# Kernel tuning notes

Hardware: AMD Instinct MI355X
Metric: run time of the kernel (lower is better)

The kernel has to match this reference:

```python
import jax, jax.numpy as jnp
import numpy as np

DIM = 4096
N_HEADS = 32
N_KV_HEADS = 8
HEAD_DIM = DIM // N_HEADS  # 128
N_REP = N_HEADS // N_KV_HEADS  # 4
MAX_BS = 16
MAX_SEQ = 4096
SEQLEN = 1
START_POS = 4095
ROPE_THETA = 500000.0


def setup_inputs() -> dict:
    key = jax.random.key(0)
    ks = jax.random.split(key, 8)
    w_scale = 0.02  # keep logits in a sane range
    x = jax.random.normal(ks[0], (MAX_BS, SEQLEN, DIM), dtype=jnp.float32)
    wq = jax.random.normal(ks[1], (DIM, N_HEADS * HEAD_DIM), dtype=jnp.float32) * w_scale
    wk = jax.random.normal(ks[2], (DIM, N_KV_HEADS * HEAD_DIM), dtype=jnp.float32) * w_scale
    wv = jax.random.normal(ks[3], (DIM, N_KV_HEADS * HEAD_DIM), dtype=jnp.float32) * w_scale
    wo = jax.random.normal(ks[4], (N_HEADS * HEAD_DIM, DIM), dtype=jnp.float32) * w_scale
    cache_k = jax.random.normal(ks[5], (MAX_BS, MAX_SEQ, N_KV_HEADS, HEAD_DIM), dtype=jnp.float32)
    cache_v = jax.random.normal(ks[6], (MAX_BS, MAX_SEQ, N_KV_HEADS, HEAD_DIM), dtype=jnp.float32)
    # true rotary frequencies for positions [START_POS, START_POS+SEQLEN)
    inv_freq = 1.0 / (ROPE_THETA ** (np.arange(0, HEAD_DIM, 2, dtype=np.float32) / HEAD_DIM))  # [hd/2]
    t = np.arange(START_POS, START_POS + SEQLEN, dtype=np.float32)[:, None]  # [s,1]
    angles = t * inv_freq[None, :]  # [s, hd/2]
    freqs_cos = jnp.asarray(np.cos(angles), dtype=jnp.float32)
    freqs_sin = jnp.asarray(np.sin(angles), dtype=jnp.float32)
    return {"x": x, "wq": wq, "wk": wk, "wv": wv, "wo": wo,
            "cache_k": cache_k, "cache_v": cache_v,
            "freqs_cos": freqs_cos, "freqs_sin": freqs_sin,
            "start_pos": START_POS}


def _rope(t, cos, sin):
    # t: [b, s, h, hd]; cos/sin: [s, hd/2] -> broadcast [1, s, 1, hd/2]
    b, s, h, hd = t.shape
    tp = t.reshape(b, s, h, hd // 2, 2)
    e, o = tp[..., 0], tp[..., 1]
    c = cos[None, :, None, :]
    sn = sin[None, :, None, :]
    re = e * c - o * sn
    im = e * sn + o * c
    return jnp.stack([re, im], axis=-1).reshape(b, s, h, hd)


def reference(x, wq, wk, wv, wo, cache_k, cache_v, freqs_cos, freqs_sin, start_pos):
    bsz, seqlen, _ = x.shape
    xq = (x @ wq).reshape(bsz, seqlen, N_HEADS, HEAD_DIM)
    xk = (x @ wk).reshape(bsz, seqlen, N_KV_HEADS, HEAD_DIM)
    xv = (x @ wv).reshape(bsz, seqlen, N_KV_HEADS, HEAD_DIM)
    xq = _rope(xq, freqs_cos, freqs_sin)
    xk = _rope(xk, freqs_cos, freqs_sin)
    # KV-cache append
    cache_k = jax.lax.dynamic_update_slice(cache_k, xk, (0, start_pos, 0, 0))
    cache_v = jax.lax.dynamic_update_slice(cache_v, xv, (0, start_pos, 0, 0))
    kv_len = start_pos + seqlen  # static Python int
    keys = cache_k[:, :kv_len]    # [b, t, g, hd]
    values = cache_v[:, :kv_len]  # [b, t, g, hd]
    # GQA via broadcasting (math-equivalent to repeat_kv)
    q = xq.reshape(bsz, seqlen, N_KV_HEADS, N_REP, HEAD_DIM)
    scale = 1.0 / jnp.sqrt(jnp.float32(HEAD_DIM))
    scores = jnp.einsum('bsgrh,btgh->bgrst', q, keys) * scale  # [b,g,r,s,t]
    probs = jax.nn.softmax(scores.astype(jnp.float32), axis=-1).astype(xq.dtype)
    out = jnp.einsum('bgrst,btgh->bsgrh', probs, values)  # [b,s,g,r,hd]
    out = out.reshape(bsz, seqlen, N_HEADS * HEAD_DIM)
    return out @ wo
```

## Files before the change

### kernel.cpp

```cpp
#include <hip/hip_runtime.h>
#include <math.h>

#define DIM    4096
#define NH     32
#define NKV    8
#define HD     128
#define BS     16
#define KVLEN  4096
#define LASTPOS 4095
#define QKV_COLS 6144
#define NKC    64

typedef float f32x4 __attribute__((ext_vector_type(4)));

#define WS_QKV   0
#define WS_ATTN  98304
#define WS_PART  163840
#define WS_PQ    4489216
#define WS_PW    10780672

__global__ __launch_bounds__(256) void qkv_projA(
    const float* __restrict__ x, const float* __restrict__ wq,
    const float* __restrict__ wk, const float* __restrict__ wv,
    float* __restrict__ pq) {
  __shared__ float xs[16 * 64];
  const int tid = threadIdx.x;
  const int col = (blockIdx.x * 256 + tid) * 2;
  const int kc = blockIdx.y;
  const int k0 = kc * 64;

  for (int i = tid; i < 1024; i += 256) {
    int b = i >> 6, k = i & 63;
    xs[i] = x[b * DIM + k0 + k];
  }
  __syncthreads();

  const float* w;
  int wstride, wcol;
  if (col < 4096)      { w = wq; wstride = 4096; wcol = col; }
  else if (col < 5120) { w = wk; wstride = 1024; wcol = col - 4096; }
  else                 { w = wv; wstride = 1024; wcol = col - 5120; }
  const float* wp = w + (size_t)k0 * wstride + wcol;

  float acc0[16], acc1[16];
#pragma unroll
  for (int b = 0; b < 16; ++b) { acc0[b] = 0.f; acc1[b] = 0.f; }

#pragma unroll 2
  for (int k = 0; k < 64; k += 4) {
    float2 w0 = *(const float2*)(wp + (size_t)(k + 0) * wstride);
    float2 w1 = *(const float2*)(wp + (size_t)(k + 1) * wstride);
    float2 w2 = *(const float2*)(wp + (size_t)(k + 2) * wstride);
    float2 w3 = *(const float2*)(wp + (size_t)(k + 3) * wstride);
#pragma unroll
    for (int b = 0; b < 16; ++b) {
      float4 xb = *(const float4*)(&xs[b * 64 + k]);
      acc0[b] += xb.x * w0.x + xb.y * w1.x + xb.z * w2.x + xb.w * w3.x;
      acc1[b] += xb.x * w0.y + xb.y * w1.y + xb.z * w2.y + xb.w * w3.y;
    }
  }
#pragma unroll
  for (int b = 0; b < 16; ++b) {
    *(float2*)(&pq[((size_t)kc * 16 + b) * QKV_COLS + col]) = make_float2(acc0[b], acc1[b]);
  }
}

__global__ __launch_bounds__(256) void qkv_projB(
    const float* __restrict__ pq, float* __restrict__ qkv,
    const float* __restrict__ fc, const float* __restrict__ fs) {
  int t = blockIdx.x * 256 + threadIdx.x;
  int b = t / 3072, pr = t % 3072;
  int col = 2 * pr;
  float e = 0.f, o = 0.f;
#pragma unroll 8
  for (int kc = 0; kc < NKC; ++kc) {
    float2 v = *(const float2*)(&pq[((size_t)kc * 16 + b) * QKV_COLS + col]);
    e += v.x; o += v.y;
  }
  float re = e, im = o;
  if (col < 5120) {
    int i = (col & 127) >> 1;
    float c = fc[i], s = fs[i];
    float scale = (col < 4096) ? 0.08838834764831845f : 1.0f;
    re = (e * c - o * s) * scale;
    im = (e * s + o * c) * scale;
  }
  *(float2*)(&qkv[b * QKV_COLS + col]) = make_float2(re, im);
}

__global__ __launch_bounds__(256) void attn_partial(
    const float* __restrict__ cache_k, const float* __restrict__ cache_v,
    const float* __restrict__ qkv, float* __restrict__ part) {
  const int tid = threadIdx.x;
  const int w = tid >> 6, lane = tid & 63;
  const int p2 = lane >> 5, ql = lane & 31;
  const int chunk = blockIdx.x & 15;
  const int bg = blockIdx.x >> 4;
  const int b = bg >> 3, g = bg & 7;
  const int t0 = chunk * 256 + w * 64;

  const float* qbase = qkv + b * QKV_COLS + g * 512;
  f32x4 qh[4];
#pragma unroll
  for (int h = 0; h < 4; ++h) qh[h] = *(const f32x4*)(qbase + h * 128 + ql * 4);

  const float* kw = cache_k + (size_t)b * 4194304 + g * 128 + (size_t)t0 * 1024;
  const float* vw = cache_v + (size_t)b * 4194304 + g * 128 + (size_t)t0 * 1024;
  const float* xk = qkv + b * QKV_COLS + 4096 + g * 128;
  const float* xv = qkv + b * QKV_COLS + 5120 + g * 128;

  float m[4], l[4];
  f32x4 acc[4];
#pragma unroll
  for (int h = 0; h < 4; ++h) { m[h] = -1e30f; l[h] = 0.f; acc[h] = (f32x4)(0.f); }

  const bool haslast = (t0 + 63 == LASTPOS);

  for (int bt = 0; bt < 8; ++bt) {
    const float* kb8 = kw + bt * 8192;
    const float* vb8 = vw + bt * 8192;
    f32x4 kf[4], vf[4];
    if (!haslast || bt < 7) {
#pragma unroll
      for (int j = 0; j < 4; ++j)
        kf[j] = *(const f32x4*)(kb8 + (2 * j + p2) * 1024 + ql * 4);
#pragma unroll
      for (int j = 0; j < 4; ++j)
        vf[j] = *(const f32x4*)(vb8 + (2 * j + p2) * 1024 + ql * 4);
    } else {
#pragma unroll
      for (int j = 0; j < 4; ++j) {
        int t = t0 + 56 + 2 * j + p2;
        const float* kr = (t == LASTPOS) ? xk : (kb8 + (2 * j + p2) * 1024);
        kf[j] = *(const f32x4*)(kr + ql * 4);
      }
#pragma unroll
      for (int j = 0; j < 4; ++j) {
        int t = t0 + 56 + 2 * j + p2;
        const float* vr = (t == LASTPOS) ? xv : (vb8 + (2 * j + p2) * 1024);
        vf[j] = *(const f32x4*)(vr + ql * 4);
      }
    }

    float sv[4][4];
#pragma unroll
    for (int j = 0; j < 4; ++j) {
#pragma unroll
      for (int h = 0; h < 4; ++h) {
        f32x4 pr = kf[j] * qh[h];
        sv[j][h] = pr[0] + pr[1] + pr[2] + pr[3];
      }
    }
#pragma unroll
    for (int off = 1; off < 32; off <<= 1) {
#pragma unroll
      for (int j = 0; j < 4; ++j) {
#pragma unroll
        for (int h = 0; h < 4; ++h)
          sv[j][h] += __shfl_xor(sv[j][h], off);
      }
    }

#pragma unroll
    for (int h = 0; h < 4; ++h) {
      float bm = fmaxf(fmaxf(sv[0][h], sv[1][h]), fmaxf(sv[2][h], sv[3][h]));
      bm = fmaxf(bm, __shfl_xor(bm, 32));
      float mn = fmaxf(m[h], bm);
      float f = __expf(m[h] - mn);
      m[h] = mn;
      acc[h] *= f;
#pragma unroll
      for (int j = 0; j < 4; ++j) sv[j][h] = __expf(sv[j][h] - mn);
      float ls = sv[0][h] + sv[1][h] + sv[2][h] + sv[3][h];
      ls += __shfl_xor(ls, 32);
      l[h] = l[h] * f + ls;
    }

#pragma unroll
    for (int j = 0; j < 4; ++j) {
#pragma unroll
      for (int h = 0; h < 4; ++h) acc[h] += sv[j][h] * vf[j];
    }
  }

#pragma unroll
  for (int h = 0; h < 4; ++h) {
#pragma unroll
    for (int k = 0; k < 4; ++k) acc[h][k] += __shfl_xor(acc[h][k], 32);
  }

  const size_t u = (size_t)blockIdx.x * 4 + w;
  if (lane < 32) {
#pragma unroll
    for (int h = 0; h < 4; ++h)
      *(f32x4*)(&part[(u * 4 + h) * 132 + ql * 4]) = acc[h];
  }
  if (lane == 0) {
#pragma unroll
    for (int h = 0; h < 4; ++h) {
      part[(u * 4 + h) * 132 + 128] = m[h];
      part[(u * 4 + h) * 132 + 129] = l[h];
    }
  }
}

__global__ __launch_bounds__(256) void attn_combine(
    const float* __restrict__ part, float* __restrict__ attn_out) {
  int t = blockIdx.x * 256 + threadIdx.x;
  int d = t & 127, h = (t >> 7) & 3, g = (t >> 9) & 7, b = t >> 12;
  int bg = b * 8 + g;
  float M = -1e30f, num = 0.f, den = 0.f;
  for (int u = 0; u < 64; ++u) {
    const float* pr = part + ((size_t)(bg * 64 + u) * 4 + h) * 132;
    float mc = pr[128];
    float Mn = fmaxf(M, mc);
    float fo = __expf(M - Mn);
    float fcur = __expf(mc - Mn);
    num = num * fo + fcur * pr[d];
    den = den * fo + fcur * pr[129];
    M = Mn;
  }
  attn_out[b * DIM + (g * 4 + h) * 128 + d] = num / den;
}

__global__ __launch_bounds__(256) void out_projA(
    const float* __restrict__ attn, const float* __restrict__ wo,
    float* __restrict__ pw) {
  __shared__ float xs[16 * 64];
  const int tid = threadIdx.x;
  const int col = (blockIdx.x * 256 + tid) * 2;
  const int kc = blockIdx.y;
  const int k0 = kc * 64;

  for (int i = tid; i < 1024; i += 256) {
    int b = i >> 6, k = i & 63;
    xs[i] = attn[b * DIM + k0 + k];
  }
  __syncthreads();

  const float* wp = wo + (size_t)k0 * 4096 + col;
  float acc0[16], acc1[16];
#pragma unroll
  for (int b = 0; b < 16; ++b) { acc0[b] = 0.f; acc1[b] = 0.f; }

#pragma unroll 2
  for (int k = 0; k < 64; k += 4) {
    float2 w0 = *(const float2*)(wp + (size_t)(k + 0) * 4096);
    float2 w1 = *(const float2*)(wp + (size_t)(k + 1) * 4096);
    float2 w2 = *(const float2*)(wp + (size_t)(k + 2) * 4096);
    float2 w3 = *(const float2*)(wp + (size_t)(k + 3) * 4096);
#pragma unroll
    for (int b = 0; b < 16; ++b) {
      float4 xb = *(const float4*)(&xs[b * 64 + k]);
      acc0[b] += xb.x * w0.x + xb.y * w1.x + xb.z * w2.x + xb.w * w3.x;
      acc1[b] += xb.x * w0.y + xb.y * w1.y + xb.z * w2.y + xb.w * w3.y;
    }
  }
#pragma unroll
  for (int b = 0; b < 16; ++b) {
    *(float2*)(&pw[((size_t)kc * 16 + b) * DIM + col]) = make_float2(acc0[b], acc1[b]);
  }
}

__global__ __launch_bounds__(256) void out_projB(
    const float* __restrict__ pw, float* __restrict__ out) {
  int t = blockIdx.x * 256 + threadIdx.x;
  int b = t >> 12, col = t & 4095;
  float sum = 0.f;
#pragma unroll 8
  for (int kc = 0; kc < NKC; ++kc)
    sum += pw[((size_t)kc * 16 + b) * DIM + col];
  out[b * DIM + col] = sum;
}

extern "C" void kernel_launch(void* const* d_in, const int* in_sizes, int n_in,
                              void* d_out, int out_size, void* d_ws, size_t ws_size,
                              hipStream_t stream) {
  const float* x  = (const float*)d_in[0];
  const float* wq = (const float*)d_in[1];
  const float* wk = (const float*)d_in[2];
  const float* wv = (const float*)d_in[3];
  const float* wo = (const float*)d_in[4];
  const float* ck = (const float*)d_in[5];
  const float* cv = (const float*)d_in[6];
  const float* fc = (const float*)d_in[7];
  const float* fs = (const float*)d_in[8];

  float* ws_f  = (float*)d_ws;
  float* qkv   = ws_f + WS_QKV;
  float* attn  = ws_f + WS_ATTN;
  float* part  = ws_f + WS_PART;
  float* pq    = ws_f + WS_PQ;
  float* pw    = ws_f + WS_PW;
  float* out   = (float*)d_out;

  qkv_projA<<<dim3(12, NKC), 256, 0, stream>>>(x, wq, wk, wv, pq);
  qkv_projB<<<192, 256, 0, stream>>>(pq, qkv, fc, fs);
  attn_partial<<<2048, 256, 0, stream>>>(ck, cv, qkv, part);
  attn_combine<<<256, 256, 0, stream>>>(part, attn);
  out_projA<<<dim3(8, NKC), 256, 0, stream>>>(attn, wo, pw);
  out_projB<<<256, 256, 0, stream>>>(pw, out);
}
```

Before: 205.4 us.

## Double-buffer KV loads and reduce warp partials in shared memory before combine

The attention partial kernel now prefetches the next K/V tile into a second register buffer while it computes on the current one, with the loop fully unrolled. This is meant to hide global-memory latency. The four per-warp softmax partials are also merged in shared memory inside each block, so only one partial per block is written. That cuts the partial buffer and the combine loop from 64 to 16 entries, and the workspace offsets shrink to match. The cost is higher register pressure from the double buffer, plus a __syncthreads and some exp work per block.

```diff
diff --git a/kernel.cpp b/kernel.cpp
--- a/kernel.cpp
+++ b/kernel.cpp
@@ -16,8 +16,8 @@
 #define WS_QKV   0
 #define WS_ATTN  98304
 #define WS_PART  163840
-#define WS_PQ    4489216
-#define WS_PW    10780672
+#define WS_PQ    1245184
+#define WS_PW    7536640
 
 __global__ __launch_bounds__(256) void qkv_projA(
     const float* __restrict__ x, const float* __restrict__ wq,
@@ -91,6 +91,7 @@
 __global__ __launch_bounds__(256) void attn_partial(
     const float* __restrict__ cache_k, const float* __restrict__ cache_v,
     const float* __restrict__ qkv, float* __restrict__ part) {
+  __shared__ float red[4][4][130];
   const int tid = threadIdx.x;
   const int w = tid >> 6, lane = tid & 63;
   const int p2 = lane >> 5, ql = lane & 31;
@@ -116,38 +117,44 @@
 
   const bool haslast = (t0 + 63 == LASTPOS);
 
+  f32x4 kf[2][4], vf[2][4];
+
+#define LOADKV(buf, bt)                                                      \
+  {                                                                          \
+    const float* kb8 = kw + (bt) * 8192;                                     \
+    const float* vb8 = vw + (bt) * 8192;                                     \
+    if (!haslast || (bt) < 7) {                                              \
+      _Pragma("unroll")                                                      \
+      for (int j = 0; j < 4; ++j)                                            \
+        kf[buf][j] = *(const f32x4*)(kb8 + (2 * j + p2) * 1024 + ql * 4);    \
+      _Pragma("unroll")                                                      \
+      for (int j = 0; j < 4; ++j)                                            \
+        vf[buf][j] = *(const f32x4*)(vb8 + (2 * j + p2) * 1024 + ql * 4);    \
+    } else {                                                                 \
+      _Pragma("unroll")                                                      \
+      for (int j = 0; j < 4; ++j) {                                          \
+        int t = t0 + 56 + 2 * j + p2;                                        \
+        const float* kr = (t == LASTPOS) ? xk : (kb8 + (2 * j + p2) * 1024); \
+        kf[buf][j] = *(const f32x4*)(kr + ql * 4);                           \
+        const float* vr = (t == LASTPOS) ? xv : (vb8 + (2 * j + p2) * 1024); \
+        vf[buf][j] = *(const f32x4*)(vr + ql * 4);                           \
+      }                                                                      \
+    }                                                                        \
+  }
+
+  LOADKV(0, 0);
+
+#pragma unroll
   for (int bt = 0; bt < 8; ++bt) {
-    const float* kb8 = kw + bt * 8192;
-    const float* vb8 = vw + bt * 8192;
-    f32x4 kf[4], vf[4];
-    if (!haslast || bt < 7) {
-#pragma unroll
-      for (int j = 0; j < 4; ++j)
-        kf[j] = *(const f32x4*)(kb8 + (2 * j + p2) * 1024 + ql * 4);
-#pragma unroll
-      for (int j = 0; j < 4; ++j)
-        vf[j] = *(const f32x4*)(vb8 + (2 * j + p2) * 1024 + ql * 4);
-    } else {
-#pragma unroll
-      for (int j = 0; j < 4; ++j) {
-        int t = t0 + 56 + 2 * j + p2;
-        const float* kr = (t == LASTPOS) ? xk : (kb8 + (2 * j + p2) * 1024);
-        kf[j] = *(const f32x4*)(kr + ql * 4);
-      }
-#pragma unroll
-      for (int j = 0; j < 4; ++j) {
-        int t = t0 + 56 + 2 * j + p2;
-        const float* vr = (t == LASTPOS) ? xv : (vb8 + (2 * j + p2) * 1024);
-        vf[j] = *(const f32x4*)(vr + ql * 4);
-      }
-    }
+    const int cur = bt & 1;
+    if (bt < 7) { LOADKV(cur ^ 1, bt + 1); }
 
     float sv[4][4];
 #pragma unroll
     for (int j = 0; j < 4; ++j) {
 #pragma unroll
       for (int h = 0; h < 4; ++h) {
-        f32x4 pr = kf[j] * qh[h];
+        f32x4 pr = kf[cur][j] * qh[h];
         sv[j][h] = pr[0] + pr[1] + pr[2] + pr[3];
       }
     }
@@ -179,9 +186,10 @@
 #pragma unroll
     for (int j = 0; j < 4; ++j) {
 #pragma unroll
-      for (int h = 0; h < 4; ++h) acc[h] += sv[j][h] * vf[j];
-    }
-  }
+      for (int h = 0; h < 4; ++h) acc[h] += sv[j][h] * vf[cur][j];
+    }
+  }
+#undef LOADKV
 
 #pragma unroll
   for (int h = 0; h < 4; ++h) {
@@ -189,29 +197,47 @@
     for (int k = 0; k < 4; ++k) acc[h][k] += __shfl_xor(acc[h][k], 32);
   }
 
-  const size_t u = (size_t)blockIdx.x * 4 + w;
   if (lane < 32) {
 #pragma unroll
     for (int h = 0; h < 4; ++h)
-      *(f32x4*)(&part[(u * 4 + h) * 132 + ql * 4]) = acc[h];
+      *(f32x4*)(&red[w][h][ql * 4]) = acc[h];
   }
   if (lane == 0) {
 #pragma unroll
     for (int h = 0; h < 4; ++h) {
-      part[(u * 4 + h) * 132 + 128] = m[h];
-      part[(u * 4 + h) * 132 + 129] = l[h];
-    }
+      red[w][h][128] = m[h];
+      red[w][h][129] = l[h];
+    }
+  }
+  __syncthreads();
+
+  for (int item = tid; item < 512; item += 256) {
+    int h = item >> 7, d = item & 127;
+    float M = -1e30f;
+#pragma unroll
+    for (int w2 = 0; w2 < 4; ++w2) M = fmaxf(M, red[w2][h][128]);
+    float num = 0.f, den = 0.f;
+#pragma unroll
+    for (int w2 = 0; w2 < 4; ++w2) {
+      float wgt = __expf(red[w2][h][128] - M);
+      num += wgt * red[w2][h][d];
+      den += wgt * red[w2][h][129];
+    }
+    size_t pi = ((size_t)blockIdx.x * 4 + h) * 132;
+    part[pi + d] = num;
+    if (d == 0) { part[pi + 128] = M; part[pi + 129] = den; }
   }
 }
 
 __global__ __launch_bounds__(256) void attn_combine(
     const float* __restrict__ part, float* __restrict__ attn_out) {
   int t = blockIdx.x * 256 + threadIdx.x;
-  int d = t & 127, h = (t >> 7) & 3, g = (t >> 9) & 7, b = t >> 12;
-  int bg = b * 8 + g;
+  int d = t & 127, h = (t >> 7) & 3, bg = t >> 9;
+  int b = bg >> 3, g = bg & 7;
   float M = -1e30f, num = 0.f, den = 0.f;
-  for (int u = 0; u < 64; ++u) {
-    const float* pr = part + ((size_t)(bg * 64 + u) * 4 + h) * 132;
+#pragma unroll 4
+  for (int c = 0; c < 16; ++c) {
+    const float* pr = part + ((size_t)(bg * 16 + c) * 4 + h) * 132;
     float mc = pr[128];
     float Mn = fmaxf(M, mc);
     float fo = __expf(M - Mn);
```

Measured after the change: 266.5 us. 1.3x slower.
